# Kernel optimization log

Hardware: AMD Instinct MI355X
Metric: run time of the kernel (lower is better)

The kernel has to match this reference:

```python
import math
import jax, jax.numpy as jnp
import numpy as np

EPS_NORM = 1e-6
EPS_COS = 1e-6


def setup_inputs() -> dict:
    key = jax.random.key(0)
    ks = jax.random.split(key, 6)
    B, C, T, H, W = 2, 768, 8, 24, 24
    d_head = 64
    nh = C // d_head  # 12
    x = jax.random.normal(ks[0], (B, C, T, H, W), jnp.float32)
    pos = jax.random.uniform(ks[1], (B, H, W, 2), jnp.float32)
    cond = jax.random.normal(ks[2], (B, C), jnp.float32)
    # NOTE: original zero-inits norm.linear and out_proj; we use small random
    # weights so the reference exercises the full math path.
    norm_w = jax.random.normal(ks[3], (C, C), jnp.float32) * 0.02
    qkv_w = jax.random.normal(ks[4], (3 * C, C), jnp.float32) * (1.0 / math.sqrt(C))
    scale = jnp.full((nh,), 10.0, jnp.float32)
    out_w = jax.random.normal(ks[5], (C, C), jnp.float32) * 0.02
    # AxialRoPE freqs buffer, exactly as in torch:
    dim = d_head // 2
    n = nh * dim // 4
    lf = np.linspace(math.log(math.pi), math.log(10.0 * math.pi), n + 1)[:-1]
    freqs = jnp.asarray(np.exp(lf).reshape(dim // 4, nh).T, jnp.float32)  # [nh, d_head//8]
    return dict(x=x, pos=pos, cond=cond, norm_w=norm_w, qkv_w=qkv_w,
                scale=scale, out_w=out_w, freqs=freqs)


def reference(x, pos, cond, norm_w, qkv_w, scale, out_w, freqs):
    B, C, T, H, W = x.shape
    nh = freqs.shape[0]
    e = C // nh
    s = H * W
    n = B * T
    skip = x

    # b c t h w -> (b t) h w c
    xr = jnp.transpose(x, (0, 2, 3, 4, 1)).reshape(n, H, W, C)
    # cond: b c -> (b t) c
    condr = jnp.repeat(cond, T, axis=0)

    # AdaRMSNorm
    cs = condr @ norm_w.T + 1.0  # [n, C]
    ms = jnp.mean(xr.astype(jnp.float32) ** 2, axis=-1, keepdims=True)
    xn = (xr * (cs[:, None, None, :] * jax.lax.rsqrt(ms + EPS_NORM))).astype(x.dtype)

    # QKV projection
    qkv = xn @ qkv_w.T  # [n, H, W, 3C]
    qkv = qkv.reshape(n, s, 3, nh, e)
    q = jnp.transpose(qkv[:, :, 0], (0, 2, 1, 3))  # [n, nh, s, e]
    k = jnp.transpose(qkv[:, :, 1], (0, 2, 1, 3))
    v = jnp.transpose(qkv[:, :, 2], (0, 2, 1, 3))

    # cosine-sim QK rescale (per-head learned scale)
    sq = jnp.sqrt(scale)[:, None, None]  # [nh,1,1]
    q = q * (sq * jax.lax.rsqrt(jnp.sum(q ** 2, axis=-1, keepdims=True) + EPS_COS))
    k = k * (sq * jax.lax.rsqrt(jnp.sum(k ** 2, axis=-1, keepdims=True) + EPS_COS))

    # axial RoPE: theta [B, s, nh, 2*dth] -> repeat over T -> [n, nh, s, d]
    posf = pos.reshape(B, s, 2)
    th = posf[:, :, 0, None, None] * freqs  # [B, s, nh, dth]
    tw = posf[:, :, 1, None, None] * freqs
    theta = jnp.concatenate([th, tw], axis=-1)
    theta = jnp.repeat(theta, T, axis=0)
    theta = jnp.transpose(theta, (0, 2, 1, 3))  # [n, nh, s, d]
    cos_t, sin_t = jnp.cos(theta), jnp.sin(theta)
    d = theta.shape[-1]

    def rot(t):
        t1, t2, rest = t[..., :d], t[..., d:2 * d], t[..., 2 * d:]
        return jnp.concatenate([t1 * cos_t - t2 * sin_t,
                                t2 * cos_t + t1 * sin_t, rest], axis=-1)

    q = rot(q)
    k = rot(k)

    # SDPA with scale=1.0
    attn = jax.nn.softmax(jnp.einsum('bhqe,bhke->bhqk', q, k), axis=-1)
    o = jnp.einsum('bhqk,bhke->bhqe', attn, v)  # [n, nh, s, e]

    # n nh (h w) e -> n h w (nh e)
    o = jnp.transpose(o, (0, 2, 1, 3)).reshape(n, H, W, C)
    o = o @ out_w.T
    # (b t) h w c -> b c t h w
    o = o.reshape(B, T, H, W, C).transpose(0, 4, 1, 2, 3)
    return o + skip
```

## Files before the change

kernel.cpp:

```cpp
#include <hip/hip_runtime.h>
#include <hip/hip_bf16.h>

#define CDIM 768
#define NHEAD 12
#define EDIM 64
#define TDIM 8
#define SDIM 576
#define NROW 16
#define MDIM 9216
#define QKVN 2304

typedef __attribute__((ext_vector_type(4))) float f32x4;
typedef __bf16 bf16x8 __attribute__((ext_vector_type(8)));
typedef unsigned short u16;
typedef __attribute__((ext_vector_type(8))) unsigned short u16x8;

__device__ inline float bf2f(u16 u) {
  union { unsigned int i; float f; } x; x.i = ((unsigned int)u) << 16; return x.f;
}
__device__ inline u16 f2bf(float f) {
  union { float f; unsigned int i; } x; x.f = f;
  unsigned int i = x.i;
  return (u16)((i + 0x7FFFu + ((i >> 16) & 1u)) >> 16);
}
__device__ inline unsigned cvt_pk_bf16(float lo, float hi) {
  unsigned r;
  asm("v_cvt_pk_bf16_f32 %0, %1, %2" : "=v"(r) : "v"(lo), "v"(hi));
  return r;
}

__global__ __launch_bounds__(256) void cs_kernel(const float* __restrict__ cond,
                                                 const float* __restrict__ nw,
                                                 float* __restrict__ cs) {
  int idx = blockIdx.x * 256 + threadIdx.x;
  int b = idx / CDIM, c = idx % CDIM;
  const float* cr = cond + (size_t)b * CDIM;
  const float* wr = nw + (size_t)c * CDIM;
  float s = 1.0f;
  for (int j = 0; j < CDIM; j += 4) {
    float4 a = *(const float4*)(cr + j);
    float4 w = *(const float4*)(wr + j);
    s = fmaf(a.x, w.x, s); s = fmaf(a.y, w.y, s);
    s = fmaf(a.z, w.z, s); s = fmaf(a.w, w.w, s);
  }
  cs[idx] = s;
}

__global__ __launch_bounds__(256) void norm_prep_kernel(const float* __restrict__ x,
                                                        const float* __restrict__ cs,
                                                        u16* __restrict__ xn,
                                                        const float* __restrict__ qkv_w,
                                                        u16* __restrict__ wq,
                                                        const float* __restrict__ out_w,
                                                        u16* __restrict__ wo,
                                                        const float* __restrict__ pos,
                                                        const float* __restrict__ freqs,
                                                        float2* __restrict__ trig) {
  __shared__ float xs[16][772];
  __shared__ float red[16][17];
  __shared__ float rfac[16];
  int bid = blockIdx.x;
  int tid = threadIdx.x;
  if (bid < 576) {
    int n = bid / 36;
    int hw0 = (bid - n * 36) * 16;
    int b = n >> 3, t = n & 7;
    int tx = tid & 15, ty = tid >> 4;
    const float* xb = x + ((size_t)b * CDIM * TDIM + t) * SDIM;
    float acc = 0.0f;
    for (int c = ty; c < CDIM; c += 16) {
      float v = xb[(size_t)c * (TDIM * SDIM) + hw0 + tx];
      xs[tx][c] = v;
      acc = fmaf(v, v, acc);
    }
    red[ty][tx] = acc;
    __syncthreads();
    if (ty == 0) {
      float s = 0.0f;
      #pragma unroll
      for (int j = 0; j < 16; j++) s += red[j][tx];
      rfac[tx] = rsqrtf(s * (1.0f / (float)CDIM) + 1e-6f);
    }
    __syncthreads();
    const float* csb = cs + (size_t)b * CDIM;
    #pragma unroll
    for (int i = 0; i < 6; i++) {
      int idx = i * 256 + tid;
      int row = idx / 96;
      int cseg = idx - row * 96;
      int c0 = cseg * 8;
      float rf = rfac[row];
      float4 a0 = *(const float4*)&xs[row][c0];
      float4 a1 = *(const float4*)&xs[row][c0 + 4];
      float4 w0 = *(const float4*)(csb + c0);
      float4 w1 = *(const float4*)(csb + c0 + 4);
      union { u16x8 v; unsigned u[4]; } ov;
      ov.u[0] = cvt_pk_bf16(a0.x * w0.x * rf, a0.y * w0.y * rf);
      ov.u[1] = cvt_pk_bf16(a0.z * w0.z * rf, a0.w * w0.w * rf);
      ov.u[2] = cvt_pk_bf16(a1.x * w1.x * rf, a1.y * w1.y * rf);
      ov.u[3] = cvt_pk_bf16(a1.z * w1.z * rf, a1.w * w1.w * rf);
      *(u16x8*)(xn + ((size_t)n * SDIM + hw0 + row) * CDIM + c0) = ov.v;
    }
  } else if (bid < 2304) {
    int i = (bid - 576) * 256 + tid;
    float4 v = *(const float4*)(qkv_w + (size_t)i * 4);
    union { unsigned long long d; unsigned u[2]; } pk;
    pk.u[0] = cvt_pk_bf16(v.x, v.y);
    pk.u[1] = cvt_pk_bf16(v.z, v.w);
    *(unsigned long long*)(wq + (size_t)i * 4) = pk.d;
  } else if (bid < 2880) {
    int i = (bid - 2304) * 256 + tid;
    float4 v = *(const float4*)(out_w + (size_t)i * 4);
    union { unsigned long long d; unsigned u[2]; } pk;
    pk.u[0] = cvt_pk_bf16(v.x, v.y);
    pk.u[1] = cvt_pk_bf16(v.z, v.w);
    *(unsigned long long*)(wo + (size_t)i * 4) = pk.d;
  } else {
    int idx = (bid - 2880) * 256 + tid;
    int j = idx & 15;
    int hb = idx >> 4;
    int h = hb / 1152;
    int bs = hb - h * 1152;
    float p = pos[(size_t)bs * 2 + (j >> 3)];
    float th = p * freqs[h * 8 + (j & 7)];
    float sn, cn;
    __sincosf(th, &sn, &cn);
    trig[idx] = make_float2(cn, sn);
  }
}

__device__ __forceinline__ void gemm_bt_lds(const u16* __restrict__ A,
                                            const u16* __restrict__ B,
                                            int K, int m0, int n0, int tid,
                                            u16* ldsA, u16* ldsB,
                                            f32x4 acc[4][4]) {
  int lane = tid & 63;
  int wid = tid >> 6;
  int wm = (wid >> 1) * 64, wn = (wid & 1) * 64;
  int lr = lane & 15, lg = lane >> 4;
  const u16* gA = A + (size_t)(m0 + wid * 32 + (lane >> 3)) * K + (((lane & 7) ^ (lane >> 3)) * 8);
  const u16* gB = B + (size_t)(n0 + wid * 32 + (lane >> 3)) * K + (((lane & 7) ^ (lane >> 3)) * 8);
  u16* dA = ldsA + wid * 2048;
  u16* dB = ldsB + wid * 2048;
  auto STAGE = [&](int buf, int k0) {
    u16* dAb = dA + buf * 8192;
    u16* dBb = dB + buf * 8192;
    #pragma unroll
    for (int is = 0; is < 4; is++) {
      __builtin_amdgcn_global_load_lds(
          (const __attribute__((address_space(1))) unsigned int*)(gA + (size_t)(is * 8) * K + k0),
          (__attribute__((address_space(3))) unsigned int*)(dAb + is * 512),
          16, 0, 0);
      __builtin_amdgcn_global_load_lds(
          (const __attribute__((address_space(1))) unsigned int*)(gB + (size_t)(is * 8) * K + k0),
          (__attribute__((address_space(3))) unsigned int*)(dBb + is * 512),
          16, 0, 0);
    }
  };
  int nt = K >> 6;
  STAGE(0, 0);
  int cur = 0;
  #pragma unroll 1
  for (int t = 0; t < nt; t++) {
    if (t + 1 < nt) {
      STAGE(cur ^ 1, (t + 1) * 64);
      asm volatile("s_waitcnt vmcnt(8)" ::: "memory");
    } else {
      asm volatile("s_waitcnt vmcnt(0)" ::: "memory");
    }
    __builtin_amdgcn_s_barrier();
    __builtin_amdgcn_sched_barrier(0);
    const u16* lA = ldsA + cur * 8192;
    const u16* lB = ldsB + cur * 8192;
    #pragma unroll
    for (int kk = 0; kk < 2; kk++) {
      bf16x8 af[4], bfr[4];
      #pragma unroll
      for (int i = 0; i < 4; i++)
        af[i]  = *(const bf16x8*)&lA[(wm + i * 16 + lr) * 64 + (((lg + 4 * kk) ^ (lr & 7)) * 8)];
      #pragma unroll
      for (int j = 0; j < 4; j++)
        bfr[j] = *(const bf16x8*)&lB[(wn + j * 16 + lr) * 64 + (((lg + 4 * kk) ^ (lr & 7)) * 8)];
      #pragma unroll
      for (int i = 0; i < 4; i++)
        #pragma unroll
        for (int j = 0; j < 4; j++)
          acc[i][j] = __builtin_amdgcn_mfma_f32_16x16x32_bf16(af[i], bfr[j], acc[i][j], 0, 0, 0);
    }
    __builtin_amdgcn_sched_barrier(0);
    __builtin_amdgcn_s_barrier();
    __builtin_amdgcn_sched_barrier(0);
    cur ^= 1;
  }
}

__device__ __forceinline__ void swz_tile(int L, int& m0, int& n0) {
  int xcd = L & 7, loc = L >> 3;
  int nblk = loc / 9, mloc = loc - nblk * 9;
  m0 = (xcd * 9 + mloc) * 128;
  n0 = nblk * 128;
}

__global__ __launch_bounds__(256) void gemm_qkv(const u16* __restrict__ xn,
                                                const u16* __restrict__ wq,
                                                const float2* __restrict__ trig,
                                                const float* __restrict__ scale,
                                                u16* __restrict__ q,
                                                u16* __restrict__ k,
                                                u16* __restrict__ vt) {
  __shared__ u16 smem[32768];
  u16* ldsA = smem;
  u16* ldsB = smem + 16384;
  f32x4 acc[4][4] = {};
  int tid = threadIdx.x;
  int m0, n0;
  swz_tile(blockIdx.x, m0, n0);
  gemm_bt_lds(xn, wq, CDIM, m0, n0, tid, ldsA, ldsB, acc);
  int lane = tid & 63, wid = tid >> 6;
  int wm = (wid >> 1) * 64, wn = (wid & 1) * 64;
  int lr = lane & 15, rb = (lane >> 4) * 4;
  int part = n0 / CDIM;
  int hbase = (n0 - part * CDIM) >> 6;
  int nidx_b = m0 / SDIM, rm0 = m0 - nidx_b * SDIM;
  u16* T = smem;
  if (part < 2) {
    int h = hbase + (wn >> 6);
    float sq = sqrtf(scale[h]) * (part == 0 ? 1.44269504f : 1.0f);
    const float2* tg = trig + (size_t)h * 1152 * 16;
    #pragma unroll
    for (int i = 0; i < 4; i++)
      #pragma unroll
      for (int r = 0; r < 4; r++) {
        int off = wm + i * 16 + rb + r;
        int sp = rm0 + off;
        int nidx = nidx_b + (sp >= SDIM);
        sp -= (sp >= SDIM) ? SDIM : 0;
        int b = nidx >> 3;
        float2 cssn = tg[((size_t)b * SDIM + sp) * 16 + lr];
        float v0 = acc[i][0][r];
        float v1 = acc[i][1][r];
        float v2 = acc[i][2][r];
        float v3 = acc[i][3][r];
        float ss = v0 * v0 + v1 * v1 + v2 * v2 + v3 * v3;
        ss += __shfl_xor(ss, 1); ss += __shfl_xor(ss, 2);
        ss += __shfl_xor(ss, 4); ss += __shfl_xor(ss, 8);
        float rs = sq * rsqrtf(ss + 1e-6f);
        v0 *= rs; v1 *= rs; v2 *= rs; v3 *= rs;
        float o0 = v0 * cssn.x - v1 * cssn.y;
        float o1 = v1 * cssn.x + v0 * cssn.y;
        u16* trow = T + (size_t)off * 136 + wn + lr;
        trow[0]  = f2bf(o0); trow[16] = f2bf(o1);
        trow[32] = f2bf(v2); trow[48] = f2bf(v3);
      }
    __syncthreads();
    u16* dst = (part == 0) ? q : k;
    #pragma unroll
    for (int c = 0; c < 8; c++) {
      int chunk = c * 256 + tid;
      int ml = chunk >> 4, sub = chunk & 15;
      int sp = rm0 + ml;
      int nidx = nidx_b + (sp >= SDIM);
      sp -= (sp >= SDIM) ? SDIM : 0;
      int hl = sub >> 3, e0 = (sub & 7) * 8;
      u16x8 v = *(const u16x8*)&T[(size_t)ml * 136 + sub * 8];
      *(u16x8*)(dst + ((size_t)(nidx * NHEAD + hbase + hl) * SDIM + sp) * EDIM + e0) = v;
    }
  } else {
    #pragma unroll
    for (int i = 0; i < 4; i++)
      #pragma unroll
      for (int j = 0; j < 4; j++)
        #pragma unroll
        for (int r = 0; r < 4; r++)
          T[(size_t)(wn + j * 16 + lr) * 136 + (wm + i * 16 + rb + r)] = f2bf(acc[i][j][r]);
    __syncthreads();
    #pragma unroll
    for (int c = 0; c < 8; c++) {
      int chunk = c * 256 + tid;
      int nl = chunk >> 4, sub = chunk & 15;
      int hl = nl >> 6, e = nl & 63;
      int hw = rm0 + sub * 8;
      int nidx = nidx_b + (hw >= SDIM);
      hw -= (hw >= SDIM) ? SDIM : 0;
      u16x8 v = *(const u16x8*)&T[(size_t)nl * 136 + sub * 8];
      *(u16x8*)(vt + ((size_t)(nidx * NHEAD + hbase + hl) * EDIM + e) * SDIM + hw) = v;
    }
  }
}

__global__ __launch_bounds__(256, 2) void attn_mfma(const u16* __restrict__ q,
                                                    const u16* __restrict__ k,
                                                    const u16* __restrict__ vt,
                                                    u16* __restrict__ o) {
  __shared__ u16 kbuf[3][4096];
  __shared__ u16 vbuf[3][4096];
  __shared__ u16 p_lds[4][48][72];
  int L = blockIdx.x;
  int cid = (L & 7) * 72 + (L >> 3);
  int nh_ = cid / 3;
  int qt = cid - nh_ * 3;
  int n = nh_ / NHEAD, h = nh_ - n * NHEAD;
  int tid = threadIdx.x;
  int wid = tid >> 6, lane = tid & 63;
  int lr = lane & 15, lg = lane >> 4;
  int qbase = qt * 192 + wid * 48;

  const u16* qp = q + ((size_t)nh_ * SDIM + qbase) * EDIM;
  bf16x8 qa[3][2];
  #pragma unroll
  for (int f = 0; f < 3; f++) {
    qa[f][0] = *(const bf16x8*)(qp + (size_t)(f * 16 + lr) * EDIM + lg * 8);
    qa[f][1] = *(const bf16x8*)(qp + (size_t)(f * 16 + lr) * EDIM + 32 + lg * 8);
  }
  const u16* kb = k + (size_t)nh_ * SDIM * EDIM;
  const u16* vb = vt + (size_t)nh_ * EDIM * SDIM;

  int srow = wid * 16 + (lane >> 3);
  int schunk = (lane & 7) ^ (lane >> 3);
  auto STAGE = [&](int buf, int s0) {
    #pragma unroll
    for (int is = 0; is < 2; is++) {
      int row = srow + is * 8;
      __builtin_amdgcn_global_load_lds(
          (const __attribute__((address_space(1))) unsigned int*)(kb + (size_t)(s0 + row) * EDIM + schunk * 8),
          (__attribute__((address_space(3))) unsigned int*)(&kbuf[buf][(size_t)(wid * 16 + is * 8 + (lane >> 3)) * 64 + (lane & 7) * 8]),
          16, 0, 0);
      __builtin_amdgcn_global_load_lds(
          (const __attribute__((address_space(1))) unsigned int*)(vb + (size_t)row * SDIM + s0 + schunk * 8),
          (__attribute__((address_space(3))) unsigned int*)(&vbuf[buf][(size_t)(wid * 16 + is * 8 + (lane >> 3)) * 64 + (lane & 7) * 8]),
          16, 0, 0);
    }
  };

  float psum[3] = {0.0f, 0.0f, 0.0f};
  f32x4 oacc[3][4] = {};

  STAGE(0, 0);
  STAGE(1, 64);
  #pragma unroll 1
  for (int kt = 0; kt < 9; kt++) {
    if (kt < 8) {
      asm volatile("s_waitcnt vmcnt(4)" ::: "memory");
    } else {
      asm volatile("s_waitcnt vmcnt(0)" ::: "memory");
    }
    __builtin_amdgcn_s_barrier();
    __builtin_amdgcn_sched_barrier(0);
    if (kt < 7) STAGE((kt + 2) % 3, (kt + 2) * 64);
    const u16* kl = kbuf[kt % 3];
    const u16* vl = vbuf[kt % 3];
    bf16x8 kf[4][2];
    #pragma unroll
    for (int j = 0; j < 4; j++) {
      kf[j][0] = *(const bf16x8*)&kl[(j * 16 + lr) * 64 + ((lg       ^ (lr & 7)) * 8)];
      kf[j][1] = *(const bf16x8*)&kl[(j * 16 + lr) * 64 + (((lg + 4) ^ (lr & 7)) * 8)];
    }
    bf16x8 vf[2][4];
    #pragma unroll
    for (int ks = 0; ks < 2; ks++)
      #pragma unroll
      for (int et = 0; et < 4; et++)
        vf[ks][et] = *(const bf16x8*)&vl[(et * 16 + lr) * 64 + (((ks * 4 + lg) ^ (lr & 7)) * 8)];
    #pragma unroll
    for (int f = 0; f < 3; f++) {
      f32x4 sfr[4] = {};
      __builtin_amdgcn_s_setprio(1);
      #pragma unroll
      for (int j = 0; j < 4; j++) {
        sfr[j] = __builtin_amdgcn_mfma_f32_16x16x32_bf16(kf[j][0], qa[f][0], sfr[j], 0, 0, 0);
        sfr[j] = __builtin_amdgcn_mfma_f32_16x16x32_bf16(kf[j][1], qa[f][1], sfr[j], 0, 0, 0);
      }
      __builtin_amdgcn_s_setprio(0);
      float fs = 0.0f;
      #pragma unroll
      for (int j = 0; j < 4; j++) {
        float p0 = exp2f(sfr[j][0]);
        float p1 = exp2f(sfr[j][1]);
        float p2 = exp2f(sfr[j][2]);
        float p3 = exp2f(sfr[j][3]);
        unsigned w0 = cvt_pk_bf16(p0, p1);
        unsigned w1 = cvt_pk_bf16(p2, p3);
        *(unsigned*)&p_lds[wid][f * 16 + lr][j * 16 + lg * 4]     = w0;
        *(unsigned*)&p_lds[wid][f * 16 + lr][j * 16 + lg * 4 + 2] = w1;
        fs += (p0 + p1) + (p2 + p3);
      }
      psum[f] += fs;
    }
    __builtin_amdgcn_s_setprio(1);
    #pragma unroll
    for (int f = 0; f < 3; f++)
      #pragma unroll
      for (int ks = 0; ks < 2; ks++) {
        bf16x8 pa = *(const bf16x8*)&p_lds[wid][f * 16 + lr][ks * 32 + lg * 8];
        #pragma unroll
        for (int et = 0; et < 4; et++)
          oacc[f][et] = __builtin_amdgcn_mfma_f32_16x16x32_bf16(pa, vf[ks][et], oacc[f][et], 0, 0, 0);
      }
    __builtin_amdgcn_s_setprio(0);
    __builtin_amdgcn_sched_barrier(0);
  }
  u16* ob = o + ((size_t)n * SDIM + qbase) * CDIM + h * EDIM;
  #pragma unroll
  for (int f = 0; f < 3; f++) {
    float s = psum[f];
    s += __shfl_xor(s, 16);
    s += __shfl_xor(s, 32);
    float inv = 1.0f / s;
    #pragma unroll
    for (int r = 0; r < 4; r++) {
      float invr = __shfl(inv, lg * 4 + r);
      #pragma unroll
      for (int et = 0; et < 4; et++)
        ob[(size_t)(f * 16 + lg * 4 + r) * CDIM + et * 16 + lr] = f2bf(oacc[f][et][r] * invr);
    }
  }
}

__global__ __launch_bounds__(256) void gemm_proj(const u16* __restrict__ o,
                                                 const u16* __restrict__ wo,
                                                 const float* __restrict__ x,
                                                 float* __restrict__ out) {
  __shared__ __align__(16) char smem[128 * 132 * 4];
  u16* ldsA = (u16*)smem;
  u16* ldsB = (u16*)smem + 16384;
  f32x4 acc[4][4] = {};
  int tid = threadIdx.x;
  int m0, n0;
  swz_tile(blockIdx.x, m0, n0);
  gemm_bt_lds(o, wo, CDIM, m0, n0, tid, ldsA, ldsB, acc);
  int lane = tid & 63, wid = tid >> 6;
  int wm = (wid >> 1) * 64, wn = (wid & 1) * 64;
  int lr = lane & 15, rb = (lane >> 4) * 4;
  int nidx_b = m0 / SDIM, rm0 = m0 - nidx_b * SDIM;
  float* T = (float*)smem;
  #pragma unroll
  for (int i = 0; i < 4; i++)
    #pragma unroll
    for (int j = 0; j < 4; j++)
      #pragma unroll
      for (int r = 0; r < 4; r++)
        T[(size_t)(wn + j * 16 + lr) * 132 + (wm + i * 16 + rb + r)] = acc[i][j][r];
  __syncthreads();
  #pragma unroll
  for (int c = 0; c < 16; c++) {
    int chunk = c * 256 + tid;
    int nl = chunk >> 5, sub = chunk & 31;
    int hw = rm0 + sub * 4;
    int nidx = nidx_b + (hw >= SDIM);
    hw -= (hw >= SDIM) ? SDIM : 0;
    int b = nidx >> 3, t = nidx & 7;
    int jj = n0 + nl;
    size_t oi = ((size_t)(b * CDIM + jj) * TDIM + t) * SDIM + hw;
    float4 xv = *(const float4*)&x[oi];
    float4 tv = *(const float4*)&T[(size_t)nl * 132 + sub * 4];
    float4 ov;
    ov.x = tv.x + xv.x; ov.y = tv.y + xv.y;
    ov.z = tv.z + xv.z; ov.w = tv.w + xv.w;
    *(float4*)&out[oi] = ov;
  }
}

extern "C" void kernel_launch(void* const* d_in, const int* in_sizes, int n_in,
                              void* d_out, int out_size, void* d_ws, size_t ws_size,
                              hipStream_t stream) {
  const float* x      = (const float*)d_in[0];
  const float* pos    = (const float*)d_in[1];
  const float* cond   = (const float*)d_in[2];
  const float* norm_w = (const float*)d_in[3];
  const float* qkv_w  = (const float*)d_in[4];
  const float* scale  = (const float*)d_in[5];
  const float* out_w  = (const float*)d_in[6];
  const float* freqs  = (const float*)d_in[7];
  float* out = (float*)d_out;

  char* ws = (char*)d_ws;
  size_t off = 0;
  auto alloc = [&](size_t bytes) -> char* {
    char* p = ws + off;
    off = (off + bytes + 255) & ~(size_t)255;
    return p;
  };
  float* cs   = (float*)alloc(2 * CDIM * sizeof(float));
  u16* wq     = (u16*)alloc((size_t)QKVN * CDIM * 2);
  u16* wo     = (u16*)alloc((size_t)CDIM * CDIM * 2);
  u16* xn     = (u16*)alloc((size_t)MDIM * CDIM * 2);
  u16* qb     = (u16*)alloc((size_t)MDIM * CDIM * 2);
  u16* kb     = (u16*)alloc((size_t)MDIM * CDIM * 2);
  u16* vt     = (u16*)alloc((size_t)MDIM * CDIM * 2);
  u16* ob     = (u16*)alloc((size_t)MDIM * CDIM * 2);
  float2* trg = (float2*)alloc((size_t)NHEAD * 2 * SDIM * 16 * sizeof(float2));

  cs_kernel<<<dim3(6), dim3(256), 0, stream>>>(cond, norm_w, cs);
  norm_prep_kernel<<<dim3(3744), dim3(256), 0, stream>>>(x, cs, xn, qkv_w, wq,
                                                         out_w, wo, pos, freqs, trg);
  gemm_qkv<<<dim3(8 * 9 * (QKVN / 128)), dim3(256), 0, stream>>>(xn, wq, trg, scale, qb, kb, vt);
  attn_mfma<<<dim3(576), dim3(256), 0, stream>>>(qb, kb, vt, ob);
  gemm_proj<<<dim3(8 * 9 * (CDIM / 128)), dim3(256), 0, stream>>>(ob, wo, x, out);
}
```

Measured before the change: 161.9 us.

## Enlarge QKV GEMM tile to 256x128 with 512 threads; split-K the cond projection

The QKV GEMM now uses 8 waves per block over a 256x128 output tile, with its own inlined global_load_lds double-buffered K loop and XOR-swizzled LDS. Because the B tile is reused across twice as many rows, it is meant to cut weight reloads and block count. The epilogue strides and V-transpose staging pitch are updated to match. Separately, the tiny cs_kernel splits each dot product over 4 lanes with shuffle reduction to expose more parallelism. The larger LDS footprint and block size may lower occupancy.

```diff
diff --git a/kernel.cpp b/kernel.cpp
--- a/kernel.cpp
+++ b/kernel.cpp
@@ -33,17 +33,21 @@
                                                  const float* __restrict__ nw,
                                                  float* __restrict__ cs) {
   int idx = blockIdx.x * 256 + threadIdx.x;
-  int b = idx / CDIM, c = idx % CDIM;
-  const float* cr = cond + (size_t)b * CDIM;
-  const float* wr = nw + (size_t)c * CDIM;
-  float s = 1.0f;
-  for (int j = 0; j < CDIM; j += 4) {
+  int out = idx >> 2, ks = idx & 3;
+  int b = out / CDIM, c = out - b * CDIM;
+  const float* cr = cond + (size_t)b * CDIM + ks * 192;
+  const float* wr = nw + (size_t)c * CDIM + ks * 192;
+  float s = 0.0f;
+  #pragma unroll
+  for (int j = 0; j < 192; j += 4) {
     float4 a = *(const float4*)(cr + j);
     float4 w = *(const float4*)(wr + j);
     s = fmaf(a.x, w.x, s); s = fmaf(a.y, w.y, s);
     s = fmaf(a.z, w.z, s); s = fmaf(a.w, w.w, s);
   }
-  cs[idx] = s;
+  s += __shfl_xor(s, 1);
+  s += __shfl_xor(s, 2);
+  if (ks == 0) cs[out] = s + 1.0f;
 }
 
 __global__ __launch_bounds__(256) void norm_prep_kernel(const float* __restrict__ x,
@@ -201,30 +205,89 @@
   n0 = nblk * 128;
 }
 
-__global__ __launch_bounds__(256) void gemm_qkv(const u16* __restrict__ xn,
+__global__ __launch_bounds__(512) void gemm_qkv(const u16* __restrict__ xn,
                                                 const u16* __restrict__ wq,
                                                 const float2* __restrict__ trig,
                                                 const float* __restrict__ scale,
                                                 u16* __restrict__ q,
                                                 u16* __restrict__ k,
                                                 u16* __restrict__ vt) {
-  __shared__ u16 smem[32768];
+  __shared__ u16 smem[49152];
   u16* ldsA = smem;
-  u16* ldsB = smem + 16384;
+  u16* ldsB = smem + 32768;
   f32x4 acc[4][4] = {};
   int tid = threadIdx.x;
-  int m0, n0;
-  swz_tile(blockIdx.x, m0, n0);
-  gemm_bt_lds(xn, wq, CDIM, m0, n0, tid, ldsA, ldsB, acc);
   int lane = tid & 63, wid = tid >> 6;
-  int wm = (wid >> 1) * 64, wn = (wid & 1) * 64;
-  int lr = lane & 15, rb = (lane >> 4) * 4;
+  int wr = wid >> 1, wc = wid & 1;
+  int wm = wr * 64, wn = wc * 64;
+  int lr = lane & 15, lg = lane >> 4;
+  int L = blockIdx.x;
+  int cid = (L & 7) * 81 + (L >> 3);
+  int mb = cid / 18, nb = cid - mb * 18;
+  int m0 = mb * 256, n0 = nb * 128;
+
+  const u16* gA = xn + (size_t)(m0 + wid * 32 + (lane >> 3)) * CDIM + (((lane & 7) ^ (lane >> 3)) * 8);
+  const u16* gB = wq + (size_t)(n0 + wid * 16 + (lane >> 3)) * CDIM + (((lane & 7) ^ (lane >> 3)) * 8);
+  u16* dA = ldsA + wid * 2048;
+  u16* dB = ldsB + wid * 1024;
+  auto STAGE = [&](int buf, int k0) {
+    u16* dAb = dA + buf * 16384;
+    u16* dBb = dB + buf * 8192;
+    #pragma unroll
+    for (int is = 0; is < 4; is++)
+      __builtin_amdgcn_global_load_lds(
+          (const __attribute__((address_space(1))) unsigned int*)(gA + (size_t)(is * 8) * CDIM + k0),
+          (__attribute__((address_space(3))) unsigned int*)(dAb + is * 512),
+          16, 0, 0);
+    #pragma unroll
+    for (int is = 0; is < 2; is++)
+      __builtin_amdgcn_global_load_lds(
+          (const __attribute__((address_space(1))) unsigned int*)(gB + (size_t)(is * 8) * CDIM + k0),
+          (__attribute__((address_space(3))) unsigned int*)(dBb + is * 512),
+          16, 0, 0);
+  };
+  STAGE(0, 0);
+  int cur = 0;
+  #pragma unroll 1
+  for (int t = 0; t < 12; t++) {
+    if (t + 1 < 12) {
+      STAGE(cur ^ 1, (t + 1) * 64);
+      asm volatile("s_waitcnt vmcnt(6)" ::: "memory");
+    } else {
+      asm volatile("s_waitcnt vmcnt(0)" ::: "memory");
+    }
+    __builtin_amdgcn_s_barrier();
+    __builtin_amdgcn_sched_barrier(0);
+    const u16* lA = ldsA + cur * 16384;
+    const u16* lB = ldsB + cur * 8192;
+    #pragma unroll
+    for (int kk = 0; kk < 2; kk++) {
+      bf16x8 af[4], bfr[4];
+      #pragma unroll
+      for (int i = 0; i < 4; i++)
+        af[i]  = *(const bf16x8*)&lA[(wm + i * 16 + lr) * 64 + (((lg + 4 * kk) ^ (lr & 7)) * 8)];
+      #pragma unroll
+      for (int j = 0; j < 4; j++)
+        bfr[j] = *(const bf16x8*)&lB[(wn + j * 16 + lr) * 64 + (((lg + 4 * kk) ^ (lr & 7)) * 8)];
+      #pragma unroll
+      for (int i = 0; i < 4; i++)
+        #pragma unroll
+        for (int j = 0; j < 4; j++)
+          acc[i][j] = __builtin_amdgcn_mfma_f32_16x16x32_bf16(af[i], bfr[j], acc[i][j], 0, 0, 0);
+    }
+    __builtin_amdgcn_sched_barrier(0);
+    __builtin_amdgcn_s_barrier();
+    __builtin_amdgcn_sched_barrier(0);
+    cur ^= 1;
+  }
+
+  int rb = lg * 4;
   int part = n0 / CDIM;
   int hbase = (n0 - part * CDIM) >> 6;
   int nidx_b = m0 / SDIM, rm0 = m0 - nidx_b * SDIM;
   u16* T = smem;
   if (part < 2) {
-    int h = hbase + (wn >> 6);
+    int h = hbase + wc;
     float sq = sqrtf(scale[h]) * (part == 0 ? 1.44269504f : 1.0f);
     const float2* tg = trig + (size_t)h * 1152 * 16;
     #pragma unroll
@@ -256,7 +319,7 @@
     u16* dst = (part == 0) ? q : k;
     #pragma unroll
     for (int c = 0; c < 8; c++) {
-      int chunk = c * 256 + tid;
+      int chunk = c * 512 + tid;
       int ml = chunk >> 4, sub = chunk & 15;
       int sp = rm0 + ml;
       int nidx = nidx_b + (sp >= SDIM);
@@ -272,17 +335,17 @@
       for (int j = 0; j < 4; j++)
         #pragma unroll
         for (int r = 0; r < 4; r++)
-          T[(size_t)(wn + j * 16 + lr) * 136 + (wm + i * 16 + rb + r)] = f2bf(acc[i][j][r]);
+          T[(size_t)(wn + j * 16 + lr) * 264 + (wm + i * 16 + rb + r)] = f2bf(acc[i][j][r]);
     __syncthreads();
     #pragma unroll
     for (int c = 0; c < 8; c++) {
-      int chunk = c * 256 + tid;
-      int nl = chunk >> 4, sub = chunk & 15;
+      int chunk = c * 512 + tid;
+      int nl = chunk >> 5, sub = chunk & 31;
       int hl = nl >> 6, e = nl & 63;
       int hw = rm0 + sub * 8;
       int nidx = nidx_b + (hw >= SDIM);
       hw -= (hw >= SDIM) ? SDIM : 0;
-      u16x8 v = *(const u16x8*)&T[(size_t)nl * 136 + sub * 8];
+      u16x8 v = *(const u16x8*)&T[(size_t)nl * 264 + sub * 8];
       *(u16x8*)(vt + ((size_t)(nidx * NHEAD + hbase + hl) * EDIM + e) * SDIM + hw) = v;
     }
   }
@@ -490,10 +553,10 @@
   u16* ob     = (u16*)alloc((size_t)MDIM * CDIM * 2);
   float2* trg = (float2*)alloc((size_t)NHEAD * 2 * SDIM * 16 * sizeof(float2));
 
-  cs_kernel<<<dim3(6), dim3(256), 0, stream>>>(cond, norm_w, cs);
+  cs_kernel<<<dim3(24), dim3(256), 0, stream>>>(cond, norm_w, cs);
   norm_prep_kernel<<<dim3(3744), dim3(256), 0, stream>>>(x, cs, xn, qkv_w, wq,
                                                          out_w, wo, pos, freqs, trg);
-  gemm_qkv<<<dim3(8 * 9 * (QKVN / 128)), dim3(256), 0, stream>>>(xn, wq, trg, scale, qb, kb, vt);
+  gemm_qkv<<<dim3(648), dim3(512), 0, stream>>>(xn, wq, trg, scale, qb, kb, vt);
   attn_mfma<<<dim3(576), dim3(256), 0, stream>>>(qb, kb, vt, ob);
   gemm_proj<<<dim3(8 * 9 * (CDIM / 128)), dim3(256), 0, stream>>>(ob, wo, x, out);
 }
```

After: 150.6 us. -7.0%, faster.
